# Kernel optimization log

Measured on AMD Instinct MI355X. Metric: run time of the kernel, lower is better.

The kernel has to match this reference:

```python
import jax, jax.numpy as jnp
import numpy as np

N = 50000      # nodes
R = 3          # relations
E = 600000     # edges per relation
D_IN, D_HID, D_OUT = 128, 256, 128


def setup_inputs() -> dict:
    key = jax.random.key(0)
    ks = jax.random.split(key, 9)
    s = 0.05  # weight scale
    x = jax.random.normal(ks[0], (N, D_IN), jnp.float32)
    src = jax.random.randint(ks[1], (R, E), 0, N, dtype=jnp.int32)
    dst = jax.random.randint(ks[2], (R, E), 0, N, dtype=jnp.int32)
    Wself1 = jax.random.normal(ks[3], (R, D_IN, D_HID), jnp.float32) * s
    Wneigh1 = jax.random.normal(ks[4], (R, D_IN, D_HID), jnp.float32) * s
    b1 = jnp.zeros((R, D_HID), jnp.float32)
    Wself2 = jax.random.normal(ks[5], (R, D_HID, D_OUT), jnp.float32) * s
    Wneigh2 = jax.random.normal(ks[6], (R, D_HID, D_OUT), jnp.float32) * s
    b2 = jnp.zeros((R, D_OUT), jnp.float32)
    return dict(x=x, src=src, dst=dst, Wself1=Wself1, Wneigh1=Wneigh1, b1=b1,
                Wself2=Wself2, Wneigh2=Wneigh2, b2=b2)


def _hetero_sage_layer(x, src, dst, Wself, Wneigh, b):
    """Sum over relations of SAGEConv(mean): fc_self(x) + fc_neigh(mean_agg(x)) + b."""
    def mean_agg(s, d):
        seg = jax.ops.segment_sum(x[s], d, num_segments=N)                # [N, d]
        deg = jax.ops.segment_sum(jnp.ones((s.shape[0],), x.dtype), d,
                                  num_segments=N)                         # [N]
        return seg / jnp.maximum(deg, 1.0)[:, None]                       # 0-indeg nodes -> 0

    mean = jax.vmap(mean_agg)(src, dst)                                   # [R, N, d_in]
    # sum_r (x @ Wself_r) = x @ sum_r Wself_r  (HeteroGraphConv aggregate='sum')
    return (x @ Wself.sum(0)
            + jnp.einsum('rnd,rdh->nh', mean, Wneigh)
            + b.sum(0))


def reference(x, src, dst, Wself1, Wneigh1, b1, Wself2, Wneigh2, b2):
    h = jax.nn.relu(_hetero_sage_layer(x, src, dst, Wself1, Wneigh1, b1))
    return _hetero_sage_layer(h, src, dst, Wself2, Wneigh2, b2)
```

## Files before the change

kernel.cpp:

```cpp
#include <hip/hip_runtime.h>
#include <hip/hip_bf16.h>
#include <cstddef>


#define NN 50000
#define RR 3
#define EE 600000
#define DIN 128
#define DHID 256
#define DOUT 128
#define NRN (RR * NN)

#define RANGE 256
#define NRANGE ((NN + RANGE - 1) / RANGE)
#define NBIN (RR * NRANGE)
#define EPB 4096
#define NBLK ((RR * EE + EPB - 1) / EPB)
#define MAXB2 4096
#define MTOT (NBIN * NBLK)

typedef __hip_bfloat16 bf16;
typedef __hip_bfloat162 bf162;
typedef unsigned short u16;
typedef __attribute__((ext_vector_type(8))) short short8;
typedef __attribute__((ext_vector_type(4))) float floatx4;

__device__ __forceinline__ void async_copy16(const void* g, void* l) {
    __builtin_amdgcn_global_load_lds((const __attribute__((address_space(1))) void*)g,
                                     (__attribute__((address_space(3))) void*)l, 16, 0, 0);
}

#define PREP_A (NN * 64)
#define PREP_B (256 * 512)
#define PREP_C (512 * 256)
#define PREP_D 384
#define PREP_TOTAL (PREP_A + PREP_B + PREP_C + PREP_D)
#define PREP_BLOCKS ((PREP_TOTAL + 255) / 256)

__global__ __launch_bounds__(256) void hist_prep(const int* __restrict__ dst,
        int* __restrict__ m,
        const float* __restrict__ x,
        const float* __restrict__ Ws1, const float* __restrict__ Wn1,
        const float* __restrict__ b1,
        const float* __restrict__ Ws2, const float* __restrict__ Wn2,
        const float* __restrict__ b2,
        bf16* __restrict__ Abig, bf16* __restrict__ B1t, bf16* __restrict__ B2t,
        float* __restrict__ bias1, float* __restrict__ bias2) {
    __shared__ int lh[NBIN];
    if (blockIdx.x < NBLK) {
        for (int i = threadIdx.x; i < NBIN; i += 256) lh[i] = 0;
        __syncthreads();
        int base = blockIdx.x * EPB;
        int lim = min(EPB, RR * EE - base);
        for (int i = threadIdx.x; i < lim; i += 256) {
            int e = base + i;
            int r = e / EE;
            int d = dst[e];
            atomicAdd(&lh[r * NRANGE + (d >> 8)], 1);
        }
        __syncthreads();
        for (int i = threadIdx.x; i < NBIN; i += 256) m[i * NBLK + blockIdx.x] = lh[i];
        return;
    }
    int idx = (blockIdx.x - NBLK) * 256 + threadIdx.x;
    if (idx < PREP_A) {
        int n = idx >> 6, c2 = idx & 63;
        float2 v = *(const float2*)&x[(size_t)n * DIN + c2 * 2];
        bf162 o; o.x = __float2bfloat16(v.x); o.y = __float2bfloat16(v.y);
        *(bf162*)&Abig[(size_t)n * 512 + c2 * 2] = o;
        return;
    }
    idx -= PREP_A;
    if (idx < PREP_B) {
        int n = idx >> 9, k = idx & 511;
        float v;
        if (k < 128) {
            v = Ws1[(size_t)k * 256 + n]
              + Ws1[(size_t)(128 + k) * 256 + n]
              + Ws1[(size_t)(256 + k) * 256 + n];
        } else {
            int q = k - 128; int r = q >> 7; int kk = q & 127;
            v = Wn1[((size_t)r * 128 + kk) * 256 + n];
        }
        B1t[(size_t)n * 512 + k] = __float2bfloat16(v);
        return;
    }
    idx -= PREP_B;
    if (idx < PREP_C) {
        int n = idx >> 8, k = idx & 255;
        float v;
        if (n < 128) {
            v = Ws2[(size_t)k * 128 + n]
              + Ws2[(size_t)(256 + k) * 128 + n]
              + Ws2[(size_t)(512 + k) * 128 + n];
        } else {
            int q = n - 128; int r = q >> 7; int nn = q & 127;
            v = Wn2[((size_t)r * 256 + k) * 128 + nn];
        }
        B2t[(size_t)n * 256 + k] = __float2bfloat16(v);
        return;
    }
    idx -= PREP_C;
    if (idx < PREP_D) {
        if (idx < 256) {
            bias1[idx] = b1[idx] + b1[256 + idx] + b1[512 + idx];
        } else {
            int j = idx - 256;
            bias2[j] = b2[j] + b2[128 + j] + b2[256 + j];
        }
    }
}

__global__ __launch_bounds__(256) void mscan_blocks(int* __restrict__ data,
        int* __restrict__ bsums, int n) {
    int t = threadIdx.x;
    int base = blockIdx.x * 1024 + t * 4;
    int v[4];
    #pragma unroll
    for (int i = 0; i < 4; ++i) v[i] = (base + i < n) ? data[base + i] : 0;
    int s = v[0] + v[1] + v[2] + v[3];
    int lane = t & 63, wid = t >> 6;
    int sc = s;
    #pragma unroll
    for (int d = 1; d < 64; d <<= 1) {
        int tt = __shfl_up(sc, d, 64);
        if (lane >= d) sc += tt;
    }
    __shared__ int wsum[4], woff[4];
    if (lane == 63) wsum[wid] = sc;
    __syncthreads();
    if (t == 0) {
        int a = 0;
        #pragma unroll
        for (int i = 0; i < 4; ++i) { woff[i] = a; a += wsum[i]; }
    }
    __syncthreads();
    int run = sc - s + woff[wid];
    #pragma unroll
    for (int i = 0; i < 4; ++i) {
        if (base + i < n) data[base + i] = run;
        run += v[i];
    }
    if (t == 255) bsums[blockIdx.x] = woff[3] + wsum[3];
}

__global__ __launch_bounds__(256) void mscan_sums(int* __restrict__ bsums, int nb) {
    int t = threadIdx.x;
    int v = (t < nb) ? bsums[t] : 0;
    int lane = t & 63, wid = t >> 6;
    int sc = v;
    #pragma unroll
    for (int d = 1; d < 64; d <<= 1) {
        int tt = __shfl_up(sc, d, 64);
        if (lane >= d) sc += tt;
    }
    __shared__ int wsum[4], woff[4];
    if (lane == 63) wsum[wid] = sc;
    __syncthreads();
    if (t == 0) {
        int a = 0;
        #pragma unroll
        for (int i = 0; i < 4; ++i) { woff[i] = a; a += wsum[i]; }
    }
    __syncthreads();
    if (t < nb) bsums[t] = sc - v + woff[wid];
}

__global__ __launch_bounds__(256) void mscan_fixup(int* __restrict__ m,
        const int* __restrict__ bsums, int* __restrict__ binbase) {
    int i = blockIdx.x * 256 + threadIdx.x;
    if (i < MTOT) {
        int v = m[i] + bsums[i >> 10];
        m[i] = v;
        int q = i / NBLK;
        if (i - q * NBLK == 0) binbase[q] = v;
    }
    if (i == 0) binbase[NBIN] = RR * EE;
}

__global__ __launch_bounds__(256) void binscatter(const int* __restrict__ src,
        const int* __restrict__ dst, const int* __restrict__ m,
        unsigned* __restrict__ ebuf) {
    __shared__ int scur[NBIN];
    for (int i = threadIdx.x; i < NBIN; i += 256) scur[i] = m[i * NBLK + blockIdx.x];
    __syncthreads();
    int base = blockIdx.x * EPB;
    int lim = min(EPB, RR * EE - base);
    for (int i = threadIdx.x; i < lim; i += 256) {
        int e = base + i;
        int r = e / EE;
        int d = dst[e];
        int pos = atomicAdd(&scur[r * NRANGE + (d >> 8)], 1);
        ebuf[pos] = ((unsigned)(d & 255) << 16) | (unsigned)src[e];
    }
}

__global__ __launch_bounds__(256) void binsort(const int* __restrict__ binbase,
        const unsigned* __restrict__ ebuf, u16* __restrict__ col,
        int* __restrict__ rowptr) {
    int b = blockIdx.x;
    int r = b / NRANGE, rb = b - r * NRANGE;
    int node0 = rb * RANGE;
    int nn = min(RANGE, NN - node0);
    int beg = binbase[b], end = binbase[b + 1];
    int cnt = min(end - beg, MAXB2);

    __shared__ unsigned eb[MAXB2];
    __shared__ u16 sb[MAXB2];
    __shared__ int lh[RANGE], lc[RANGE];
    __shared__ int wsum[4], woff[4];

    for (int i = threadIdx.x; i < cnt; i += 256) eb[i] = ebuf[beg + i];
    lh[threadIdx.x] = 0;
    __syncthreads();
    for (int i = threadIdx.x; i < cnt; i += 256) atomicAdd(&lh[eb[i] >> 16], 1);
    __syncthreads();
    {
        int t = threadIdx.x, lane = t & 63, wid = t >> 6;
        int v = lh[t];
        int sc = v;
        #pragma unroll
        for (int d = 1; d < 64; d <<= 1) {
            int tt = __shfl_up(sc, d, 64);
            if (lane >= d) sc += tt;
        }
        if (lane == 63) wsum[wid] = sc;
        __syncthreads();
        if (t == 0) {
            int a = 0;
            #pragma unroll
            for (int i = 0; i < 4; ++i) { woff[i] = a; a += wsum[i]; }
        }
        __syncthreads();
        int excl = sc - v + woff[wid];
        lc[t] = excl;
        if (t < nn) rowptr[r * NN + node0 + t] = beg + excl;
        if (t == 0) rowptr[r * NN + node0 + nn] = end;
    }
    __syncthreads();
    for (int i = threadIdx.x; i < cnt; i += 256) {
        unsigned e = eb[i];
        int pos = atomicAdd(&lc[e >> 16], 1);
        sb[pos] = (u16)(e & 0xffffu);
    }
    __syncthreads();
    for (int i = threadIdx.x; i < cnt; i += 256) col[beg + i] = sb[i];
}

__device__ __forceinline__ float bflo(unsigned u) { return __uint_as_float(u << 16); }
__device__ __forceinline__ float bfhi(unsigned u) { return __uint_as_float(u & 0xffff0000u); }

__global__ __launch_bounds__(256) void gather1(const int* __restrict__ rowptr,
        const u16* __restrict__ col, bf16* __restrict__ Abig) {
    int g = blockIdx.x * 4 + (threadIdx.x >> 6);
    int lane = threadIdx.x & 63;
    int r = g / NN;
    int n = g - r * NN;
    int beg = rowptr[g], end = rowptr[g + 1];
    const unsigned* xb = (const unsigned*)Abig;
    float acc0 = 0.f, acc1 = 0.f;
    for (int base = beg; base < end; base += 64) {
        int cnt = min(64, end - base);
        int cidx = (lane < cnt) ? (int)col[base + lane] : 0;
        int j = 0;
        for (; j + 8 <= cnt; j += 8) {
            const unsigned* p0 = xb + (size_t)__builtin_amdgcn_readlane(cidx, j)     * 256;
            const unsigned* p1 = xb + (size_t)__builtin_amdgcn_readlane(cidx, j + 1) * 256;
            const unsigned* p2 = xb + (size_t)__builtin_amdgcn_readlane(cidx, j + 2) * 256;
            const unsigned* p3 = xb + (size_t)__builtin_amdgcn_readlane(cidx, j + 3) * 256;
            const unsigned* p4 = xb + (size_t)__builtin_amdgcn_readlane(cidx, j + 4) * 256;
            const unsigned* p5 = xb + (size_t)__builtin_amdgcn_readlane(cidx, j + 5) * 256;
            const unsigned* p6 = xb + (size_t)__builtin_amdgcn_readlane(cidx, j + 6) * 256;
            const unsigned* p7 = xb + (size_t)__builtin_amdgcn_readlane(cidx, j + 7) * 256;
            unsigned u0 = p0[lane], u1 = p1[lane], u2 = p2[lane], u3 = p3[lane];
            unsigned u4 = p4[lane], u5 = p5[lane], u6 = p6[lane], u7 = p7[lane];
            acc0 += bflo(u0) + bflo(u1) + bflo(u2) + bflo(u3)
                  + bflo(u4) + bflo(u5) + bflo(u6) + bflo(u7);
            acc1 += bfhi(u0) + bfhi(u1) + bfhi(u2) + bfhi(u3)
                  + bfhi(u4) + bfhi(u5) + bfhi(u6) + bfhi(u7);
        }
        for (; j + 4 <= cnt; j += 4) {
            const unsigned* p0 = xb + (size_t)__builtin_amdgcn_readlane(cidx, j)     * 256;
            const unsigned* p1 = xb + (size_t)__builtin_amdgcn_readlane(cidx, j + 1) * 256;
            const unsigned* p2 = xb + (size_t)__builtin_amdgcn_readlane(cidx, j + 2) * 256;
            const unsigned* p3 = xb + (size_t)__builtin_amdgcn_readlane(cidx, j + 3) * 256;
            unsigned u0 = p0[lane], u1 = p1[lane], u2 = p2[lane], u3 = p3[lane];
            acc0 += bflo(u0) + bflo(u1) + bflo(u2) + bflo(u3);
            acc1 += bfhi(u0) + bfhi(u1) + bfhi(u2) + bfhi(u3);
        }
        for (; j < cnt; ++j) {
            const unsigned* p = xb + (size_t)__builtin_amdgcn_readlane(cidx, j) * 256;
            unsigned u = p[lane];
            acc0 += bflo(u);
            acc1 += bfhi(u);
        }
    }
    float inv = 1.0f / fmaxf((float)(end - beg), 1.0f);
    bf162 o;
    o.x = __float2bfloat16(acc0 * inv);
    o.y = __float2bfloat16(acc1 * inv);
    *(bf162*)&Abig[(size_t)n * 512 + 128 + r * 128 + lane * 2] = o;
}

__global__ __launch_bounds__(256) void gemm1m(const bf16* __restrict__ A,
        const bf16* __restrict__ Bt, const float* __restrict__ bias1,
        bf16* __restrict__ h) {
    __shared__ short As[128 * 32];
    __shared__ short Bs[128 * 32];
    const int t = threadIdx.x;
    const int wv = t >> 6, lane = t & 63;
    const int wr = wv >> 1, wc = wv & 1;
    const int m16 = lane & 15, kg = lane >> 4;
    const int row0 = blockIdx.x * 128;
    const int col0 = blockIdx.y * 128;
    const int ldrow = (t >> 2);
    const int ldk = (t & 3) * 8;
    const int arow0 = min(row0 + ldrow, NN - 1);
    const int arow1 = min(row0 + ldrow + 64, NN - 1);
    const short* Ag0 = (const short*)A + (size_t)arow0 * 512 + ldk;
    const short* Ag1 = (const short*)A + (size_t)arow1 * 512 + ldk;
    const short* Bg = (const short*)Bt + (size_t)(col0 + ldrow) * 512 + ldk;
    short* AsW = &As[(size_t)wv * 512];
    short* BsW = &Bs[(size_t)wv * 512];

    floatx4 acc[4][4] = {};
    for (int kb = 0; kb < 512; kb += 32) {
        async_copy16(Ag0 + kb, AsW);
        async_copy16(Ag1 + kb, AsW + 2048);
        async_copy16(Bg + kb, BsW);
        async_copy16(Bg + kb + (size_t)64 * 512, BsW + 2048);
        __syncthreads();
        short8 a[4], b[4];
        #pragma unroll
        for (int i = 0; i < 4; ++i)
            a[i] = *(const short8*)&As[(wr * 64 + i * 16 + m16) * 32 + kg * 8];
        #pragma unroll
        for (int j = 0; j < 4; ++j)
            b[j] = *(const short8*)&Bs[(wc * 64 + j * 16 + m16) * 32 + kg * 8];
        #pragma unroll
        for (int i = 0; i < 4; ++i)
            #pragma unroll
            for (int j = 0; j < 4; ++j)
                acc[i][j] = __builtin_amdgcn_mfma_f32_16x16x32_bf16(a[i], b[j], acc[i][j], 0, 0, 0);
        __syncthreads();
    }
    #pragma unroll
    for (int j = 0; j < 4; ++j) {
        int c = col0 + wc * 64 + j * 16 + m16;
        float bj = bias1[c];
        #pragma unroll
        for (int i = 0; i < 4; ++i) {
            int rb = row0 + wr * 64 + i * 16 + kg * 4;
            #pragma unroll
            for (int reg = 0; reg < 4; ++reg) {
                int r = rb + reg;
                if (r < NN)
                    h[(size_t)r * DHID + c] = __float2bfloat16(fmaxf(acc[i][j][reg] + bj, 0.f));
            }
        }
    }
}

__global__ __launch_bounds__(256) void gemm2m(const bf16* __restrict__ A,
        const bf16* __restrict__ Bt, const float* __restrict__ bias2,
        float* __restrict__ out, bf16* __restrict__ y) {
    __shared__ short As[128 * 32];
    __shared__ short Bs[128 * 32];
    const int t = threadIdx.x;
    const int wv = t >> 6, lane = t & 63;
    const int wr = wv >> 1, wc = wv & 1;
    const int m16 = lane & 15, kg = lane >> 4;
    const int row0 = blockIdx.x * 128;
    const int col0 = blockIdx.y * 128;
    const int ldrow = (t >> 2);
    const int ldk = (t & 3) * 8;
    const int arow0 = min(row0 + ldrow, NN - 1);
    const int arow1 = min(row0 + ldrow + 64, NN - 1);
    const short* Ag0 = (const short*)A + (size_t)arow0 * 256 + ldk;
    const short* Ag1 = (const short*)A + (size_t)arow1 * 256 + ldk;
    const short* Bg = (const short*)Bt + (size_t)(col0 + ldrow) * 256 + ldk;
    short* AsW = &As[(size_t)wv * 512];
    short* BsW = &Bs[(size_t)wv * 512];

    floatx4 acc[4][4] = {};
    for (int kb = 0; kb < 256; kb += 32) {
        async_copy16(Ag0 + kb, AsW);
        async_copy16(Ag1 + kb, AsW + 2048);
        async_copy16(Bg + kb, BsW);
        async_copy16(Bg + kb + (size_t)64 * 256, BsW + 2048);
        __syncthreads();
        short8 a[4], b[4];
        #pragma unroll
        for (int i = 0; i < 4; ++i)
            a[i] = *(const short8*)&As[(wr * 64 + i * 16 + m16) * 32 + kg * 8];
        #pragma unroll
        for (int j = 0; j < 4; ++j)
            b[j] = *(const short8*)&Bs[(wc * 64 + j * 16 + m16) * 32 + kg * 8];
        #pragma unroll
        for (int i = 0; i < 4; ++i)
            #pragma unroll
            for (int j = 0; j < 4; ++j)
                acc[i][j] = __builtin_amdgcn_mfma_f32_16x16x32_bf16(a[i], b[j], acc[i][j], 0, 0, 0);
        __syncthreads();
    }
    if (blockIdx.y == 0) {
        #pragma unroll
        for (int j = 0; j < 4; ++j) {
            int c = wc * 64 + j * 16 + m16;
            float bj = bias2[c];
            #pragma unroll
            for (int i = 0; i < 4; ++i) {
                int rb = row0 + wr * 64 + i * 16 + kg * 4;
                #pragma unroll
                for (int reg = 0; reg < 4; ++reg) {
                    int r = rb + reg;
                    if (r < NN) out[(size_t)r * DOUT + c] = acc[i][j][reg] + bj;
                }
            }
        }
    } else {
        int rel = blockIdx.y - 1;
        bf16* yr = y + (size_t)rel * NN * DOUT;
        #pragma unroll
        for (int j = 0; j < 4; ++j) {
            int c = wc * 64 + j * 16 + m16;
            #pragma unroll
            for (int i = 0; i < 4; ++i) {
                int rb = row0 + wr * 64 + i * 16 + kg * 4;
                #pragma unroll
                for (int reg = 0; reg < 4; ++reg) {
                    int r = rb + reg;
                    if (r < NN) yr[(size_t)r * DOUT + c] = __float2bfloat16(acc[i][j][reg]);
                }
            }
        }
    }
}

__global__ __launch_bounds__(256) void gather2(const bf16* __restrict__ y,
        const int* __restrict__ rowptr, const u16* __restrict__ col,
        float* __restrict__ out) {
    int n = blockIdx.x * 4 + (threadIdx.x >> 6);
    int lane = threadIdx.x & 63;
    float2 acc = *(float2*)&out[(size_t)n * DOUT + lane * 2];
    const unsigned* yb = (const unsigned*)y;
    #pragma unroll
    for (int r = 0; r < RR; ++r) {
        const unsigned* ybr = yb + (size_t)r * NN * 64;
        int g = r * NN + n;
        int beg = rowptr[g], end = rowptr[g + 1];
        float a0 = 0.f, a1 = 0.f;
        for (int base = beg; base < end; base += 64) {
            int cnt = min(64, end - base);
            int cidx = (lane < cnt) ? (int)col[base + lane] : 0;
            int j = 0;
            for (; j + 8 <= cnt; j += 8) {
                const unsigned* p0 = ybr + (size_t)__builtin_amdgcn_readlane(cidx, j)     * 64;
                const unsigned* p1 = ybr + (size_t)__builtin_amdgcn_readlane(cidx, j + 1) * 64;
                const unsigned* p2 = ybr + (size_t)__builtin_amdgcn_readlane(cidx, j + 2) * 64;
                const unsigned* p3 = ybr + (size_t)__builtin_amdgcn_readlane(cidx, j + 3) * 64;
                const unsigned* p4 = ybr + (size_t)__builtin_amdgcn_readlane(cidx, j + 4) * 64;
                const unsigned* p5 = ybr + (size_t)__builtin_amdgcn_readlane(cidx, j + 5) * 64;
                const unsigned* p6 = ybr + (size_t)__builtin_amdgcn_readlane(cidx, j + 6) * 64;
                const unsigned* p7 = ybr + (size_t)__builtin_amdgcn_readlane(cidx, j + 7) * 64;
                unsigned u0 = p0[lane], u1 = p1[lane], u2 = p2[lane], u3 = p3[lane];
                unsigned u4 = p4[lane], u5 = p5[lane], u6 = p6[lane], u7 = p7[lane];
                a0 += bflo(u0) + bflo(u1) + bflo(u2) + bflo(u3)
                    + bflo(u4) + bflo(u5) + bflo(u6) + bflo(u7);
                a1 += bfhi(u0) + bfhi(u1) + bfhi(u2) + bfhi(u3)
                    + bfhi(u4) + bfhi(u5) + bfhi(u6) + bfhi(u7);
            }
            for (; j + 4 <= cnt; j += 4) {
                const unsigned* p0 = ybr + (size_t)__builtin_amdgcn_readlane(cidx, j)     * 64;
                const unsigned* p1 = ybr + (size_t)__builtin_amdgcn_readlane(cidx, j + 1) * 64;
                const unsigned* p2 = ybr + (size_t)__builtin_amdgcn_readlane(cidx, j + 2) * 64;
                const unsigned* p3 = ybr + (size_t)__builtin_amdgcn_readlane(cidx, j + 3) * 64;
                unsigned u0 = p0[lane], u1 = p1[lane], u2 = p2[lane], u3 = p3[lane];
                a0 += bflo(u0) + bflo(u1) + bflo(u2) + bflo(u3);
                a1 += bfhi(u0) + bfhi(u1) + bfhi(u2) + bfhi(u3);
            }
            for (; j < cnt; ++j) {
                const unsigned* p = ybr + (size_t)__builtin_amdgcn_readlane(cidx, j) * 64;
                unsigned u = p[lane];
                a0 += bflo(u);
                a1 += bfhi(u);
            }
        }
        float inv = 1.0f / fmaxf((float)(end - beg), 1.0f);
        acc.x += a0 * inv;
        acc.y += a1 * inv;
    }
    *(float2*)&out[(size_t)n * DOUT + lane * 2] = acc;
}

extern "C" void kernel_launch(void* const* d_in, const int* in_sizes, int n_in,
                              void* d_out, int out_size, void* d_ws, size_t ws_size,
                              hipStream_t stream) {
    const float* x       = (const float*)d_in[0];
    const int*   src     = (const int*)  d_in[1];
    const int*   dst     = (const int*)  d_in[2];
    const float* Wself1  = (const float*)d_in[3];
    const float* Wneigh1 = (const float*)d_in[4];
    const float* b1      = (const float*)d_in[5];
    const float* Wself2  = (const float*)d_in[6];
    const float* Wneigh2 = (const float*)d_in[7];
    const float* b2      = (const float*)d_in[8];
    float* out = (float*)d_out;

    char* ws = (char*)d_ws;
    int*      mtx     = (int*)     (ws + 0x0000000ull);
    int*      binbase = (int*)     (ws + 0x0110000ull);
    int*      bsums   = (int*)     (ws + 0x0120000ull);
    int*      rowptr  = (int*)     (ws + 0x0140000ull);
    float*    bias1   = (float*)   (ws + 0x01E1000ull);
    float*    bias2   = (float*)   (ws + 0x01E2000ull);
    unsigned* ebuf    = (unsigned*)(ws + 0x0200000ull);
    bf16*     B1t     = (bf16*)    (ws + 0x0A00000ull);
    bf16*     B2t     = (bf16*)    (ws + 0x0A40000ull);
    bf16*     Abig    = (bf16*)    (ws + 0x0B00000ull);
    bf16*     y       = (bf16*)    (ws + 0x0B00000ull);
    bf16*     h       = (bf16*)    (ws + 0x3C00000ull);
    u16*      col     = (u16*)     (ws + 0x5600000ull);

    hist_prep<<<NBLK + PREP_BLOCKS, 256, 0, stream>>>(
        dst, mtx, x, Wself1, Wneigh1, b1, Wself2, Wneigh2, b2,
        Abig, B1t, B2t, bias1, bias2);

    mscan_blocks<<<(MTOT + 1023) / 1024, 256, 0, stream>>>(mtx, bsums, MTOT);
    mscan_sums<<<1, 256, 0, stream>>>(bsums, (MTOT + 1023) / 1024);
    mscan_fixup<<<(MTOT + 255) / 256, 256, 0, stream>>>(mtx, bsums, binbase);
    binscatter<<<NBLK, 256, 0, stream>>>(src, dst, mtx, ebuf);
    binsort<<<NBIN, 256, 0, stream>>>(binbase, ebuf, col, rowptr);

    gather1<<<NRN / 4, 256, 0, stream>>>(rowptr, col, Abig);

    gemm1m<<<dim3((NN + 127) / 128, 2), 256, 0, stream>>>(Abig, B1t, bias1, h);
    gemm2m<<<dim3((NN + 127) / 128, 4), 256, 0, stream>>>(h, B2t, bias2, out, y);

    gather2<<<NN / 4, 256, 0, stream>>>(y, rowptr, col, out);
}
```

Before: 348.7 us.

## Fuse both GEMMs per row tile, keeping hidden activations in LDS

Merges gemm1m and gemm2m into one kernel. Each 128-row block computes the full 256-wide hidden tile, applies bias and ReLU, keeps it in shared memory, then runs the second GEMM from LDS. The y outputs are written in place over the block's own Abig rows using a tiled packed layout, and gather2 indexes that layout. This drops the global round-trip of h and one launch. In exchange, B weights are read directly from global memory without LDS staging, the LDS footprint grows (about 66KB for hT), and the grid is half as large as gemm1m's, which may lower occupancy.

```diff
diff --git a/kernel.cpp b/kernel.cpp
--- a/kernel.cpp
+++ b/kernel.cpp
@@ -302,167 +302,154 @@
     *(bf162*)&Abig[(size_t)n * 512 + 128 + r * 128 + lane * 2] = o;
 }
 
-__global__ __launch_bounds__(256) void gemm1m(const bf16* __restrict__ A,
-        const bf16* __restrict__ Bt, const float* __restrict__ bias1,
-        bf16* __restrict__ h) {
+__global__ __launch_bounds__(256) void gemm12(bf16* AY,
+        const bf16* __restrict__ B1t, const bf16* __restrict__ B2t,
+        const float* __restrict__ bias1, const float* __restrict__ bias2,
+        float* __restrict__ out) {
+    __shared__ bf16 hT[128 * 264];
     __shared__ short As[128 * 32];
-    __shared__ short Bs[128 * 32];
     const int t = threadIdx.x;
     const int wv = t >> 6, lane = t & 63;
     const int wr = wv >> 1, wc = wv & 1;
     const int m16 = lane & 15, kg = lane >> 4;
-    const int row0 = blockIdx.x * 128;
-    const int col0 = blockIdx.y * 128;
-    const int ldrow = (t >> 2);
-    const int ldk = (t & 3) * 8;
+    const int s = blockIdx.x;
+    const int row0 = s * 128;
+    const int ldrow = t >> 2, ldk = (t & 3) * 8;
     const int arow0 = min(row0 + ldrow, NN - 1);
     const int arow1 = min(row0 + ldrow + 64, NN - 1);
-    const short* Ag0 = (const short*)A + (size_t)arow0 * 512 + ldk;
-    const short* Ag1 = (const short*)A + (size_t)arow1 * 512 + ldk;
-    const short* Bg = (const short*)Bt + (size_t)(col0 + ldrow) * 512 + ldk;
+    const short* Ag0 = (const short*)AY + (size_t)arow0 * 512 + ldk;
+    const short* Ag1 = (const short*)AY + (size_t)arow1 * 512 + ldk;
     short* AsW = &As[(size_t)wv * 512];
-    short* BsW = &Bs[(size_t)wv * 512];
-
-    floatx4 acc[4][4] = {};
+    const short* B1s = (const short*)B1t;
+    const short* B2s = (const short*)B2t;
+
+    floatx4 acc1[2][4][4] = {};
     for (int kb = 0; kb < 512; kb += 32) {
         async_copy16(Ag0 + kb, AsW);
         async_copy16(Ag1 + kb, AsW + 2048);
-        async_copy16(Bg + kb, BsW);
-        async_copy16(Bg + kb + (size_t)64 * 512, BsW + 2048);
-        __syncthreads();
-        short8 a[4], b[4];
+        __syncthreads();
+        short8 a[4];
         #pragma unroll
         for (int i = 0; i < 4; ++i)
             a[i] = *(const short8*)&As[(wr * 64 + i * 16 + m16) * 32 + kg * 8];
         #pragma unroll
-        for (int j = 0; j < 4; ++j)
-            b[j] = *(const short8*)&Bs[(wc * 64 + j * 16 + m16) * 32 + kg * 8];
-        #pragma unroll
-        for (int i = 0; i < 4; ++i)
+        for (int ch = 0; ch < 2; ++ch) {
+            short8 b[4];
             #pragma unroll
             for (int j = 0; j < 4; ++j)
-                acc[i][j] = __builtin_amdgcn_mfma_f32_16x16x32_bf16(a[i], b[j], acc[i][j], 0, 0, 0);
+                b[j] = *(const short8*)&B1s[(size_t)(ch * 128 + wc * 64 + j * 16 + m16) * 512 + kb + kg * 8];
+            #pragma unroll
+            for (int i = 0; i < 4; ++i)
+                #pragma unroll
+                for (int j = 0; j < 4; ++j)
+                    acc1[ch][i][j] = __builtin_amdgcn_mfma_f32_16x16x32_bf16(a[i], b[j], acc1[ch][i][j], 0, 0, 0);
+        }
         __syncthreads();
     }
     #pragma unroll
-    for (int j = 0; j < 4; ++j) {
-        int c = col0 + wc * 64 + j * 16 + m16;
-        float bj = bias1[c];
-        #pragma unroll
-        for (int i = 0; i < 4; ++i) {
-            int rb = row0 + wr * 64 + i * 16 + kg * 4;
-            #pragma unroll
-            for (int reg = 0; reg < 4; ++reg) {
-                int r = rb + reg;
-                if (r < NN)
-                    h[(size_t)r * DHID + c] = __float2bfloat16(fmaxf(acc[i][j][reg] + bj, 0.f));
-            }
-        }
-    }
-}
-
-__global__ __launch_bounds__(256) void gemm2m(const bf16* __restrict__ A,
-        const bf16* __restrict__ Bt, const float* __restrict__ bias2,
-        float* __restrict__ out, bf16* __restrict__ y) {
-    __shared__ short As[128 * 32];
-    __shared__ short Bs[128 * 32];
-    const int t = threadIdx.x;
-    const int wv = t >> 6, lane = t & 63;
-    const int wr = wv >> 1, wc = wv & 1;
-    const int m16 = lane & 15, kg = lane >> 4;
-    const int row0 = blockIdx.x * 128;
-    const int col0 = blockIdx.y * 128;
-    const int ldrow = (t >> 2);
-    const int ldk = (t & 3) * 8;
-    const int arow0 = min(row0 + ldrow, NN - 1);
-    const int arow1 = min(row0 + ldrow + 64, NN - 1);
-    const short* Ag0 = (const short*)A + (size_t)arow0 * 256 + ldk;
-    const short* Ag1 = (const short*)A + (size_t)arow1 * 256 + ldk;
-    const short* Bg = (const short*)Bt + (size_t)(col0 + ldrow) * 256 + ldk;
-    short* AsW = &As[(size_t)wv * 512];
-    short* BsW = &Bs[(size_t)wv * 512];
-
-    floatx4 acc[4][4] = {};
-    for (int kb = 0; kb < 256; kb += 32) {
-        async_copy16(Ag0 + kb, AsW);
-        async_copy16(Ag1 + kb, AsW + 2048);
-        async_copy16(Bg + kb, BsW);
-        async_copy16(Bg + kb + (size_t)64 * 256, BsW + 2048);
-        __syncthreads();
-        short8 a[4], b[4];
-        #pragma unroll
-        for (int i = 0; i < 4; ++i)
-            a[i] = *(const short8*)&As[(wr * 64 + i * 16 + m16) * 32 + kg * 8];
-        #pragma unroll
-        for (int j = 0; j < 4; ++j)
-            b[j] = *(const short8*)&Bs[(wc * 64 + j * 16 + m16) * 32 + kg * 8];
-        #pragma unroll
-        for (int i = 0; i < 4; ++i)
-            #pragma unroll
-            for (int j = 0; j < 4; ++j)
-                acc[i][j] = __builtin_amdgcn_mfma_f32_16x16x32_bf16(a[i], b[j], acc[i][j], 0, 0, 0);
-        __syncthreads();
-    }
-    if (blockIdx.y == 0) {
+    for (int ch = 0; ch < 2; ++ch)
         #pragma unroll
         for (int j = 0; j < 4; ++j) {
-            int c = wc * 64 + j * 16 + m16;
-            float bj = bias2[c];
+            int c = ch * 128 + wc * 64 + j * 16 + m16;
+            float bj = bias1[c];
             #pragma unroll
             for (int i = 0; i < 4; ++i) {
-                int rb = row0 + wr * 64 + i * 16 + kg * 4;
+                int rl = wr * 64 + i * 16 + kg * 4;
                 #pragma unroll
-                for (int reg = 0; reg < 4; ++reg) {
-                    int r = rb + reg;
-                    if (r < NN) out[(size_t)r * DOUT + c] = acc[i][j][reg] + bj;
+                for (int reg = 0; reg < 4; ++reg)
+                    hT[(rl + reg) * 264 + c] =
+                        __float2bfloat16(fmaxf(acc1[ch][i][j][reg] + bj, 0.f));
+            }
+        }
+    __syncthreads();
+
+    #pragma unroll 1
+    for (int ct = 0; ct < 4; ++ct) {
+        floatx4 acc[4][4] = {};
+        for (int kb = 0; kb < 256; kb += 32) {
+            short8 a[4], b[4];
+            #pragma unroll
+            for (int i = 0; i < 4; ++i)
+                a[i] = *(const short8*)&((const short*)hT)[(wr * 64 + i * 16 + m16) * 264 + kb + kg * 8];
+            #pragma unroll
+            for (int j = 0; j < 4; ++j)
+                b[j] = *(const short8*)&B2s[(size_t)(ct * 128 + wc * 64 + j * 16 + m16) * 256 + kb + kg * 8];
+            #pragma unroll
+            for (int i = 0; i < 4; ++i)
+                #pragma unroll
+                for (int j = 0; j < 4; ++j)
+                    acc[i][j] = __builtin_amdgcn_mfma_f32_16x16x32_bf16(a[i], b[j], acc[i][j], 0, 0, 0);
+        }
+        if (ct == 0) {
+            #pragma unroll
+            for (int j = 0; j < 4; ++j) {
+                int c = wc * 64 + j * 16 + m16;
+                float bj = bias2[c];
+                #pragma unroll
+                for (int i = 0; i < 4; ++i) {
+                    int rl = wr * 64 + i * 16 + kg * 4;
+                    #pragma unroll
+                    for (int reg = 0; reg < 4; ++reg) {
+                        int r = row0 + rl + reg;
+                        if (r < NN) out[(size_t)r * DOUT + c] = acc[i][j][reg] + bj;
+                    }
                 }
             }
-        }
-    } else {
-        int rel = blockIdx.y - 1;
-        bf16* yr = y + (size_t)rel * NN * DOUT;
-        #pragma unroll
-        for (int j = 0; j < 4; ++j) {
-            int c = wc * 64 + j * 16 + m16;
-            #pragma unroll
-            for (int i = 0; i < 4; ++i) {
-                int rb = row0 + wr * 64 + i * 16 + kg * 4;
+        } else {
+            int rel = ct - 1;
+            bf16* yp = AY + ((size_t)s << 16) + ((size_t)rel << 14);
+            #pragma unroll
+            for (int j = 0; j < 4; ++j) {
+                int c = wc * 64 + j * 16 + m16;
                 #pragma unroll
-                for (int reg = 0; reg < 4; ++reg) {
-                    int r = rb + reg;
-                    if (r < NN) yr[(size_t)r * DOUT + c] = __float2bfloat16(acc[i][j][reg]);
+                for (int i = 0; i < 4; ++i) {
+                    int rl = wr * 64 + i * 16 + kg * 4;
+                    #pragma unroll
+                    for (int reg = 0; reg < 4; ++reg) {
+                        if (row0 + rl + reg < NN)
+                            yp[((rl + reg) << 7) + c] = __float2bfloat16(acc[i][j][reg]);
+                    }
                 }
             }
         }
-    }
-}
-
-__global__ __launch_bounds__(256) void gather2(const bf16* __restrict__ y,
+        __syncthreads();
+    }
+}
+
+__global__ __launch_bounds__(256) void gather2(const bf16* __restrict__ ypack,
         const int* __restrict__ rowptr, const u16* __restrict__ col,
         float* __restrict__ out) {
     int n = blockIdx.x * 4 + (threadIdx.x >> 6);
     int lane = threadIdx.x & 63;
     float2 acc = *(float2*)&out[(size_t)n * DOUT + lane * 2];
-    const unsigned* yb = (const unsigned*)y;
+    const unsigned* yb = (const unsigned*)ypack;
     #pragma unroll
     for (int r = 0; r < RR; ++r) {
-        const unsigned* ybr = yb + (size_t)r * NN * 64;
         int g = r * NN + n;
         int beg = rowptr[g], end = rowptr[g + 1];
         float a0 = 0.f, a1 = 0.f;
+        const size_t rbase = (size_t)r << 13;
         for (int base = beg; base < end; base += 64) {
             int cnt = min(64, end - base);
             int cidx = (lane < cnt) ? (int)col[base + lane] : 0;
             int j = 0;
             for (; j + 8 <= cnt; j += 8) {
-                const unsigned* p0 = ybr + (size_t)__builtin_amdgcn_readlane(cidx, j)     * 64;
-                const unsigned* p1 = ybr + (size_t)__builtin_amdgcn_readlane(cidx, j + 1) * 64;
-                const unsigned* p2 = ybr + (size_t)__builtin_amdgcn_readlane(cidx, j + 2) * 64;
-                const unsigned* p3 = ybr + (size_t)__builtin_amdgcn_readlane(cidx, j + 3) * 64;
-                const unsigned* p4 = ybr + (size_t)__builtin_amdgcn_readlane(cidx, j + 4) * 64;
-                const unsigned* p5 = ybr + (size_t)__builtin_amdgcn_readlane(cidx, j + 5) * 64;
-                const unsigned* p6 = ybr + (size_t)__builtin_amdgcn_readlane(cidx, j + 6) * 64;
-                const unsigned* p7 = ybr + (size_t)__builtin_amdgcn_readlane(cidx, j + 7) * 64;
+                int s0 = __builtin_amdgcn_readlane(cidx, j);
+                int s1 = __builtin_amdgcn_readlane(cidx, j + 1);
+                int s2 = __builtin_amdgcn_readlane(cidx, j + 2);
+                int s3 = __builtin_amdgcn_readlane(cidx, j + 3);
+                int s4 = __builtin_amdgcn_readlane(cidx, j + 4);
+                int s5 = __builtin_amdgcn_readlane(cidx, j + 5);
+                int s6 = __builtin_amdgcn_readlane(cidx, j + 6);
+                int s7 = __builtin_amdgcn_readlane(cidx, j + 7);
+                const unsigned* p0 = yb + rbase + ((size_t)(s0 >> 7) << 15) + ((s0 & 127) << 6);
+                const unsigned* p1 = yb + rbase + ((size_t)(s1 >> 7) << 15) + ((s1 & 127) << 6);
+                const unsigned* p2 = yb + rbase + ((size_t)(s2 >> 7) << 15) + ((s2 & 127) << 6);
+                const unsigned* p3 = yb + rbase + ((size_t)(s3 >> 7) << 15) + ((s3 & 127) << 6);
+                const unsigned* p4 = yb + rbase + ((size_t)(s4 >> 7) << 15) + ((s4 & 127) << 6);
+                const unsigned* p5 = yb + rbase + ((size_t)(s5 >> 7) << 15) + ((s5 & 127) << 6);
+                const unsigned* p6 = yb + rbase + ((size_t)(s6 >> 7) << 15) + ((s6 & 127) << 6);
+                const unsigned* p7 = yb + rbase + ((size_t)(s7 >> 7) << 15) + ((s7 & 127) << 6);
                 unsigned u0 = p0[lane], u1 = p1[lane], u2 = p2[lane], u3 = p3[lane];
                 unsigned u4 = p4[lane], u5 = p5[lane], u6 = p6[lane], u7 = p7[lane];
                 a0 += bflo(u0) + bflo(u1) + bflo(u2) + bflo(u3)
@@ -470,17 +457,9 @@
                 a1 += bfhi(u0) + bfhi(u1) + bfhi(u2) + bfhi(u3)
                     + bfhi(u4) + bfhi(u5) + bfhi(u6) + bfhi(u7);
             }
-            for (; j + 4 <= cnt; j += 4) {
-                const unsigned* p0 = ybr + (size_t)__builtin_amdgcn_readlane(cidx, j)     * 64;
-                const unsigned* p1 = ybr + (size_t)__builtin_amdgcn_readlane(cidx, j + 1) * 64;
-                const unsigned* p2 = ybr + (size_t)__builtin_amdgcn_readlane(cidx, j + 2) * 64;
-                const unsigned* p3 = ybr + (size_t)__builtin_amdgcn_readlane(cidx, j + 3) * 64;
-                unsigned u0 = p0[lane], u1 = p1[lane], u2 = p2[lane], u3 = p3[lane];
-                a0 += bflo(u0) + bflo(u1) + bflo(u2) + bflo(u3);
-                a1 += bfhi(u0) + bfhi(u1) + bfhi(u2) + bfhi(u3);
-            }
             for (; j < cnt; ++j) {
-                const unsigned* p = ybr + (size_t)__builtin_amdgcn_readlane(cidx, j) * 64;
+                int sj = __builtin_amdgcn_readlane(cidx, j);
+                const unsigned* p = yb + rbase + ((size_t)(sj >> 7) << 15) + ((sj & 127) << 6);
                 unsigned u = p[lane];
                 a0 += bflo(u);
                 a1 += bfhi(u);
@@ -518,8 +497,6 @@
     bf16*     B1t     = (bf16*)    (ws + 0x0A00000ull);
     bf16*     B2t     = (bf16*)    (ws + 0x0A40000ull);
     bf16*     Abig    = (bf16*)    (ws + 0x0B00000ull);
-    bf16*     y       = (bf16*)    (ws + 0x0B00000ull);
-    bf16*     h       = (bf16*)    (ws + 0x3C00000ull);
     u16*      col     = (u16*)     (ws + 0x5600000ull);
 
     hist_prep<<<NBLK + PREP_BLOCKS, 256, 0, stream>>>(
@@ -534,8 +511,7 @@
 
     gather1<<<NRN / 4, 256, 0, stream>>>(rowptr, col, Abig);
 
-    gemm1m<<<dim3((NN + 127) / 128, 2), 256, 0, stream>>>(Abig, B1t, bias1, h);
-    gemm2m<<<dim3((NN + 127) / 128, 4), 256, 0, stream>>>(h, B2t, bias2, out, y);
-
-    gather2<<<NN / 4, 256, 0, stream>>>(y, rowptr, col, out);
-}
+    gemm12<<<(NN + 127) / 128, 256, 0, stream>>>(Abig, B1t, B2t, bias1, bias2, out);
+
+    gather2<<<NN / 4, 256, 0, stream>>>(Abig, rowptr, col, out);
+}
```

New measurement: 385.3 us. 10.5% more time.
